# Performance work log

Hardware: AMD Instinct MI355X
Metric: run time of the kernel (lower is better)

## Reference

```python
import jax, jax.numpy as jnp
import numpy as np

B, L, D_MODEL = 8, 2048, 256
D_STATE, D_CONV, EXPAND, DT_RANK = 8, 4, 2, 2
D_INNER = EXPAND * D_MODEL
CHUNK = 32  # chunkSize in _parallelScan


def setup_inputs() -> dict:
    key = jax.random.key(0)
    ks = jax.random.split(key, 8)
    def nrm(k, shape, fan_in):
        return jax.random.normal(k, shape, jnp.float32) / np.float32(np.sqrt(fan_in))
    x = jax.random.normal(ks[0], (B, L, D_MODEL), jnp.float32)
    W_in = nrm(ks[1], (D_MODEL, 2 * D_INNER), D_MODEL)            # inProj (no bias)
    conv_w = nrm(ks[2], (D_INNER, 1, D_CONV), D_CONV)             # depthwise conv [O,I/g,K]
    conv_b = jnp.zeros((D_INNER,), jnp.float32)
    W_x = nrm(ks[3], (D_INNER, DT_RANK + 2 * D_STATE), D_INNER)   # xProj (no bias)
    dt_std = DT_RANK ** -0.5
    W_dt = jax.random.uniform(ks[4], (DT_RANK, D_INNER), jnp.float32, -dt_std, dt_std)
    u = jax.random.uniform(ks[5], (D_INNER,), jnp.float32)
    b_dt = u * np.float32(np.log(0.1) - np.log(0.001)) + np.float32(np.log(0.001))  # log(invDt)
    A_log = jnp.log(jnp.tile(jnp.arange(1, D_STATE + 1, dtype=jnp.float32), (D_INNER, 1)))
    Dp = jnp.ones((D_INNER,), jnp.float32)
    W_out = nrm(ks[6], (D_INNER, D_MODEL), D_INNER)
    pre_g = jnp.ones((D_MODEL,), jnp.float32)
    pre_b = jnp.zeros((D_MODEL,), jnp.float32)
    post_g = jnp.ones((D_MODEL,), jnp.float32)
    post_b = jnp.zeros((D_MODEL,), jnp.float32)
    return dict(x=x, pre_g=pre_g, pre_b=pre_b, post_g=post_g, post_b=post_b,
                W_in=W_in, conv_w=conv_w, conv_b=conv_b, W_x=W_x, W_dt=W_dt,
                b_dt=b_dt, A_log=A_log, Dp=Dp, W_out=W_out)


def layernorm(x, g, b, eps=1e-5):
    mu = jnp.mean(x, axis=-1, keepdims=True)
    var = jnp.var(x, axis=-1, keepdims=True)
    return (x - mu) * jax.lax.rsqrt(var + eps) * g + b


def _parallel_scan(deltaA, deltaBX, C, Dp, xc):
    # deltaA, deltaBX: [B, L, I, N]; C: [B, L, N]; xc: [B, L, I]
    Bb, Lb, I, N = deltaA.shape
    nC = Lb // CHUNK
    def chunked(t):
        return jnp.moveaxis(t.reshape((Bb, nC, CHUNK) + t.shape[2:]), 1, 0)
    cA, cBX, cC, cX = chunked(deltaA), chunked(deltaBX), chunked(C), chunked(xc)

    def body(h, inp):
        a, bx, c, xck = inp  # a,bx: [B,CHUNK,I,N]; c: [B,CHUNK,N]; xck: [B,CHUNK,I]
        logA = jnp.log(jnp.maximum(a, 1e-6))
        cum = jnp.cumsum(logA, axis=1)
        cumA = jnp.exp(jnp.minimum(cum, 20.0))
        hInit = h[:, None] * cumA
        inv = jnp.exp(-jnp.clip(cum, -20.0, 20.0))
        cumBX = jnp.cumsum(bx * inv, axis=1)
        hChunk = hInit + cumA * cumBX                      # [B,CHUNK,I,N]
        y = jnp.einsum('blin,bln->bli', hChunk, c) + xck * Dp
        return hChunk[:, -1], y

    h0 = jnp.zeros((Bb, I, N), deltaA.dtype)
    _, ys = jax.lax.scan(body, h0, (cA, cBX, cC, cX))      # ys: [nC,B,CHUNK,I]
    return jnp.moveaxis(ys, 0, 1).reshape(Bb, Lb, I)


def _ssm(x, W_in, conv_w, conv_b, W_x, W_dt, b_dt, A_log, Dp, W_out):
    Bb, Lb, _ = x.shape
    xr = x @ W_in                                          # [B,L,2I]
    xc, res = xr[..., :D_INNER], xr[..., D_INNER:]
    # depthwise causal conv (pad dConv-1 left == torch pad-both then slice [:L])
    xt = jnp.swapaxes(xc, 1, 2)                            # [B,I,L]
    xt = jax.lax.conv_general_dilated(
        xt, conv_w, window_strides=(1,), padding=[(D_CONV - 1, 0)],
        dimension_numbers=('NCH', 'OIH', 'NCH'), feature_group_count=D_INNER)
    xt = xt + conv_b[None, :, None]
    xc = jax.nn.silu(jnp.swapaxes(xt, 1, 2))               # [B,L,I]
    A = -jnp.exp(A_log.astype(jnp.float32))                # [I,N]
    xdbl = xc @ W_x
    delta = xdbl[..., :DT_RANK]
    Bm = xdbl[..., DT_RANK:DT_RANK + D_STATE]
    Cm = xdbl[..., DT_RANK + D_STATE:]
    delta = jax.nn.softplus(delta @ W_dt + b_dt)           # [B,L,I]
    deltaA = jnp.exp(delta[..., None] * A)                 # [B,L,I,N]
    deltaBX = delta[..., None] * Bm[:, :, None, :] * xc[..., None]
    y = _parallel_scan(deltaA, deltaBX, Cm, Dp.astype(jnp.float32), xc)
    y = y * jax.nn.silu(res)
    return y @ W_out


def reference(x, pre_g, pre_b, post_g, post_b, W_in, conv_w, conv_b, W_x, W_dt,
              b_dt, A_log, Dp, W_out):
    residual = x
    xn = layernorm(x, pre_g, pre_b)
    args = (W_in, conv_w, conv_b, W_x, W_dt, b_dt, A_log, Dp, W_out)
    h_fwd = _ssm(xn, *args)
    h_bwd = jnp.flip(_ssm(jnp.flip(xn, axis=1), *args), axis=1)
    out = residual + h_fwd + h_bwd                         # DropPath is identity (eval / p=0)
    return layernorm(out, post_g, post_b)
```

## Files before the change

### kernel.cpp

```cpp
#include <hip/hip_runtime.h>
#include <hip/hip_bf16.h>
#include <math.h>

#define BQ 8
#define LQ 2048
#define DM 256
#define DI 512
#define NS 8
#define NT (BQ*LQ)
#define NCH 64
#define CHK 32

typedef __attribute__((ext_vector_type(8))) __bf16 bf16x8;
typedef __attribute__((ext_vector_type(4))) float f32x4;

#define GPTR(p) ((const __attribute__((address_space(1))) void*)(p))
#define SPTR(p) ((__attribute__((address_space(3))) void*)(p))

__device__ __forceinline__ float fast_silu(float v){
  return v * __builtin_amdgcn_rcpf(1.0f + __expf(-v));
}
__device__ __forceinline__ unsigned short f2bf(float f){
  unsigned int u = __float_as_uint(f);
  unsigned int r = (u + 0x7FFFu + ((u >> 16) & 1u)) >> 16;
  return (unsigned short)r;
}
__device__ __forceinline__ float b2f(unsigned short u){
  return __uint_as_float(((unsigned int)u) << 16);
}
__device__ __forceinline__ f32x4 sp4(float x){ return (f32x4){x,x,x,x}; }

__global__ __launch_bounds__(256) void prep_kernel(const float* __restrict__ W_in,
                                                   const float* __restrict__ W_out,
                                                   const float* __restrict__ W_x,
                                                   unsigned short* __restrict__ WinT,
                                                   unsigned short* __restrict__ WoutT,
                                                   unsigned short* __restrict__ WxBC,
                                                   float* __restrict__ Wdt01){
  int id = blockIdx.x*256 + threadIdx.x;
  if(id < 1024*256){ int n = id >> 8, k = id & 255; WinT[id]  = f2bf(W_in[k*1024+n]); }
  if(id < 256*512){  int n = id >> 9, k = id & 511; WoutT[id] = f2bf(W_out[k*256+n]); }
  if(id < 16*512){   int j = id >> 9, k = id & 511; WxBC[id]  = f2bf(W_x[k*18+2+j]); }
  if(id < 2*512){    int j = id >> 9, k = id & 511; Wdt01[id] = W_x[k*18+j]; }
}

template<bool OB>
__global__ __launch_bounds__(256) void ln_kernel(const float* __restrict__ in,
                                                 const float* __restrict__ g,
                                                 const float* __restrict__ bv,
                                                 void* __restrict__ outp){
  int w = threadIdx.x >> 6, lane = threadIdx.x & 63;
  size_t row = (size_t)blockIdx.x*4 + w;
  const float4* rp = (const float4*)(in + row*DM);
  float4 v = rp[lane];
  float s  = v.x+v.y+v.z+v.w;
  float sq = v.x*v.x+v.y*v.y+v.z*v.z+v.w*v.w;
  #pragma unroll
  for(int m=32;m>=1;m>>=1){ s += __shfl_xor(s,m); sq += __shfl_xor(sq,m); }
  float mean = s*(1.0f/DM);
  float var  = sq*(1.0f/DM) - mean*mean;
  float rstd = rsqrtf(var + 1e-5f);
  float4 gv = ((const float4*)g)[lane];
  float4 bb = ((const float4*)bv)[lane];
  float4 o;
  o.x = (v.x-mean)*rstd*gv.x + bb.x;
  o.y = (v.y-mean)*rstd*gv.y + bb.y;
  o.z = (v.z-mean)*rstd*gv.z + bb.z;
  o.w = (v.w-mean)*rstd*gv.w + bb.w;
  if(OB){
    ushort4 q; q.x=f2bf(o.x); q.y=f2bf(o.y); q.z=f2bf(o.z); q.w=f2bf(o.w);
    *(ushort4*)((unsigned short*)outp + row*DM + lane*4) = q;
  } else {
    ((float4*)((float*)outp + row*DM))[lane] = o;
  }
}

template<int K, bool RESID, bool OUTBF>
__global__ __launch_bounds__(256) void gemm_bf16(const unsigned short* __restrict__ A,
                                                 const unsigned short* __restrict__ Bt,
                                                 const float* __restrict__ xres,
                                                 void* __restrict__ Cv, int N){
  __shared__ unsigned short As[128*32];
  __shared__ unsigned short Bs[128*32];
  const int tid = threadIdx.x;
  const int wid = tid >> 6, lane = tid & 63;
  const int wm = wid >> 1, wn = wid & 1;
  const int row0 = blockIdx.y*128, col0 = blockIdx.x*128;
  f32x4 acc[4][4] = {};

  for(int kt = 0; kt < K; kt += 32){
    {
      int ch = tid;
      const unsigned short* ga = A + (size_t)(row0 + (ch>>2))*K + kt + (ch&3)*8;
      __builtin_amdgcn_global_load_lds(GPTR(ga), SPTR(As + wid*512), 16, 0, 0);
      const unsigned short* gb = Bt + (size_t)(col0 + (ch>>2))*K + kt + (ch&3)*8;
      __builtin_amdgcn_global_load_lds(GPTR(gb), SPTR(Bs + wid*512), 16, 0, 0);
    }
    {
      int ch = tid + 256;
      const unsigned short* ga = A + (size_t)(row0 + (ch>>2))*K + kt + (ch&3)*8;
      __builtin_amdgcn_global_load_lds(GPTR(ga), SPTR(As + 2048 + wid*512), 16, 0, 0);
      const unsigned short* gb = Bt + (size_t)(col0 + (ch>>2))*K + kt + (ch&3)*8;
      __builtin_amdgcn_global_load_lds(GPTR(gb), SPTR(Bs + 2048 + wid*512), 16, 0, 0);
    }
    __syncthreads();

    bf16x8 af[4], bfv[4];
    #pragma unroll
    for(int m=0;m<4;m++)
      af[m] = *(const bf16x8*)(const void*)&As[(wm*64 + m*16 + (lane&15))*32 + (lane>>4)*8];
    #pragma unroll
    for(int n=0;n<4;n++)
      bfv[n] = *(const bf16x8*)(const void*)&Bs[(wn*64 + n*16 + (lane&15))*32 + (lane>>4)*8];
    #pragma unroll
    for(int m=0;m<4;m++)
      #pragma unroll
      for(int n=0;n<4;n++)
        acc[m][n] = __builtin_amdgcn_mfma_f32_16x16x32_bf16(af[m], bfv[n], acc[m][n], 0, 0, 0);
    __syncthreads();
  }

  const int cr = (lane>>4)*4, cc = lane&15;
  #pragma unroll
  for(int m=0;m<4;m++){
    #pragma unroll
    for(int n=0;n<4;n++){
      int col = col0 + wn*64 + n*16 + cc;
      size_t base = (size_t)(row0 + wm*64 + m*16 + cr)*N + col;
      #pragma unroll
      for(int r=0;r<4;r++){
        float v = acc[m][n][r];
        if constexpr (OUTBF){
          ((unsigned short*)Cv)[base + (size_t)r*N] = f2bf(v);
        } else {
          if constexpr (RESID) v += xres[base + (size_t)r*N];
          ((float*)Cv)[base + (size_t)r*N] = v;
        }
      }
    }
  }
}

__global__ __launch_bounds__(256) void conv_dt_kernel(const unsigned short* __restrict__ xrb,
                                                      const float* __restrict__ cw,
                                                      const float* __restrict__ cb,
                                                      const float* __restrict__ Wdt01,
                                                      float* __restrict__ xcf,
                                                      float* __restrict__ xcb,
                                                      unsigned short* __restrict__ xbf_f,
                                                      unsigned short* __restrict__ xbf_b,
                                                      float* __restrict__ dt2f,
                                                      float* __restrict__ dt2b){
  const int tid = threadIdx.x;
  const int tok = tid >> 7, q = tid & 127;
  const int i = q*4;
  const size_t row = (size_t)blockIdx.x*2 + tok;
  const int l = (int)(row & (LQ-1));

  float4 wc0 = *(const float4*)&cw[(i+0)*4];
  float4 wc1 = *(const float4*)&cw[(i+1)*4];
  float4 wc2 = *(const float4*)&cw[(i+2)*4];
  float4 wc3 = *(const float4*)&cw[(i+3)*4];
  float4 bias = *(const float4*)&cb[i];

  float4 r[7];
  #pragma unroll
  for(int d=0; d<7; d++){
    int off = d-3;
    bool ok = (l+off >= 0) && (l+off < LQ);
    if(ok){
      ushort4 t4 = *(const ushort4*)&xrb[(row+off)*1024 + i];
      r[d] = make_float4(b2f(t4.x), b2f(t4.y), b2f(t4.z), b2f(t4.w));
    } else r[d] = make_float4(0.f,0.f,0.f,0.f);
  }
  float4 sf = bias;
  sf.x += r[0].x*wc0.x + r[1].x*wc0.y + r[2].x*wc0.z + r[3].x*wc0.w;
  sf.y += r[0].y*wc1.x + r[1].y*wc1.y + r[2].y*wc1.z + r[3].y*wc1.w;
  sf.z += r[0].z*wc2.x + r[1].z*wc2.y + r[2].z*wc2.z + r[3].z*wc2.w;
  sf.w += r[0].w*wc3.x + r[1].w*wc3.y + r[2].w*wc3.z + r[3].w*wc3.w;
  float4 sb = bias;
  sb.x += r[6].x*wc0.x + r[5].x*wc0.y + r[4].x*wc0.z + r[3].x*wc0.w;
  sb.y += r[6].y*wc1.x + r[5].y*wc1.y + r[4].y*wc1.z + r[3].y*wc1.w;
  sb.z += r[6].z*wc2.x + r[5].z*wc2.y + r[4].z*wc2.z + r[3].z*wc2.w;
  sb.w += r[6].w*wc3.x + r[5].w*wc3.y + r[4].w*wc3.z + r[3].w*wc3.w;

  float4 of, ob;
  of.x = fast_silu(sf.x); of.y = fast_silu(sf.y); of.z = fast_silu(sf.z); of.w = fast_silu(sf.w);
  ob.x = fast_silu(sb.x); ob.y = fast_silu(sb.y); ob.z = fast_silu(sb.z); ob.w = fast_silu(sb.w);

  size_t e = row*512 + i;
  *(float4*)&xcf[e] = of;
  *(float4*)&xcb[e] = ob;
  ushort4 obf; obf.x=f2bf(of.x); obf.y=f2bf(of.y); obf.z=f2bf(of.z); obf.w=f2bf(of.w);
  *(ushort4*)&xbf_f[e] = obf;
  ushort4 obb; obb.x=f2bf(ob.x); obb.y=f2bf(ob.y); obb.z=f2bf(ob.z); obb.w=f2bf(ob.w);
  *(ushort4*)&xbf_b[e] = obb;

  float4 w0q = *(const float4*)&Wdt01[i];
  float4 w1q = *(const float4*)&Wdt01[512+i];
  float s0f = of.x*w0q.x + of.y*w0q.y + of.z*w0q.z + of.w*w0q.w;
  float s1f = of.x*w1q.x + of.y*w1q.y + of.z*w1q.z + of.w*w1q.w;
  float s0b = ob.x*w0q.x + ob.y*w0q.y + ob.z*w0q.z + ob.w*w0q.w;
  float s1b = ob.x*w1q.x + ob.y*w1q.y + ob.z*w1q.z + ob.w*w1q.w;
  #pragma unroll
  for(int m=32;m>=1;m>>=1){
    s0f += __shfl_xor(s0f,m); s1f += __shfl_xor(s1f,m);
    s0b += __shfl_xor(s0b,m); s1b += __shfl_xor(s1b,m);
  }
  __shared__ float red[4][4];
  int wid = tid >> 6;
  if((tid & 63) == 0){ red[wid][0]=s0f; red[wid][1]=s1f; red[wid][2]=s0b; red[wid][3]=s1b; }
  __syncthreads();
  if(tid == 0){
    size_t r0 = (size_t)blockIdx.x*2;
    dt2f[r0*2+0] = red[0][0]+red[1][0];  dt2f[r0*2+1] = red[0][1]+red[1][1];
    dt2b[r0*2+0] = red[0][2]+red[1][2];  dt2b[r0*2+1] = red[0][3]+red[1][3];
  }
  if(tid == 128){
    size_t r1 = (size_t)blockIdx.x*2 + 1;
    dt2f[r1*2+0] = red[2][0]+red[3][0];  dt2f[r1*2+1] = red[2][1]+red[3][1];
    dt2b[r1*2+0] = red[2][2]+red[3][2];  dt2b[r1*2+1] = red[2][3]+red[3][3];
  }
}

__global__ __launch_bounds__(256) void bc_gemm(const unsigned short* __restrict__ xbf_f,
                                               const unsigned short* __restrict__ xbf_b,
                                               const unsigned short* __restrict__ WxBC,
                                               float* __restrict__ BCf,
                                               float* __restrict__ BCb){
  int dir = blockIdx.y;
  const unsigned short* A = dir ? xbf_b : xbf_f;
  float* BC = dir ? BCb : BCf;
  const int row0 = blockIdx.x*256;
  __shared__ unsigned short As[256*32];
  __shared__ unsigned short Bs[16*32];
  const int tid = threadIdx.x, wid = tid>>6, lane = tid&63;
  f32x4 acc[4] = {};
  for(int kt=0; kt<512; kt+=32){
    #pragma unroll
    for(int r=0;r<4;r++){
      int ch = r*256 + tid;
      const unsigned short* ga = A + (size_t)(row0 + (ch>>2))*512 + kt + (ch&3)*8;
      __builtin_amdgcn_global_load_lds(GPTR(ga), SPTR(As + r*2048 + wid*512), 16, 0, 0);
    }
    if(wid==0){
      int ch = lane;
      const unsigned short* gb = WxBC + (size_t)(ch>>2)*512 + kt + (ch&3)*8;
      __builtin_amdgcn_global_load_lds(GPTR(gb), SPTR(Bs), 16, 0, 0);
    }
    __syncthreads();
    bf16x8 bfv = *(const bf16x8*)(const void*)&Bs[(lane&15)*32 + (lane>>4)*8];
    #pragma unroll
    for(int m=0;m<4;m++){
      bf16x8 af = *(const bf16x8*)(const void*)&As[(wid*64 + m*16 + (lane&15))*32 + (lane>>4)*8];
      acc[m] = __builtin_amdgcn_mfma_f32_16x16x32_bf16(af, bfv, acc[m], 0, 0, 0);
    }
    __syncthreads();
  }
  const int cr = (lane>>4)*4, cc = lane&15;
  #pragma unroll
  for(int m=0;m<4;m++)
    #pragma unroll
    for(int r=0;r<4;r++)
      BC[(size_t)(row0 + wid*64 + m*16 + cr + r)*16 + cc] = acc[m][r];
}

#define INV_CAP  4.85165195e8f

__global__ __launch_bounds__(256) void scan_pass1(
    const float* __restrict__ dt2f, const float* __restrict__ dt2b,
    const float* __restrict__ BCf,  const float* __restrict__ BCb,
    const float* __restrict__ xcf,  const float* __restrict__ xcb,
    const float* __restrict__ Wdt,  const float* __restrict__ bdt,
    float* __restrict__ a_arr, float* __restrict__ b_arr){
  int dir = blockIdx.z, b = blockIdx.y;
  int chunk = blockIdx.x >> 1, ib = blockIdx.x & 1;
  int i = ib*256 + threadIdx.x;
  const float* dt2 = dir ? dt2b : dt2f;
  const float* BC  = dir ? BCb  : BCf;
  const float* xc  = dir ? xcb  : xcf;
  float w0 = Wdt[i], w1 = Wdt[512+i], bd = bdt[i];
  f32x4 cAA = sp4(1.f), cAB = sp4(1.f), ivA = sp4(1.f), ivB = sp4(1.f);
  f32x4 cxA = sp4(0.f), cxB = sp4(0.f);
  for(int t=0;t<CHK;t++){
    int p = chunk*CHK + t;
    int l = dir ? (LQ-1-p) : p;
    size_t row = (size_t)b*LQ + l;
    float d0 = dt2[row*2+0], d1 = dt2[row*2+1];
    float dpre = d0*w0 + d1*w1 + bd;
    float t0 = __expf(fminf(dpre, 80.f));
    float ep = 1.f + t0;
    float e1 = __builtin_amdgcn_rcpf(ep);
    float delta = __logf(ep);
    float dxv = delta * xc[row*512+i];
    const f32x4* bc4 = (const f32x4*)&BC[row*16];
    f32x4 bmA = bc4[0], bmB = bc4[1];
    float e2=e1*e1, e4=e2*e2;
    f32x4 pdA = {e1, e2, e2*e1, e4};
    f32x4 pdB = pdA * e4;
    float g2=ep*ep, g4=g2*g2;
    f32x4 puA = {ep, g2, g2*ep, g4};
    f32x4 puB = puA * g4;
    cAA *= __builtin_elementwise_max(pdA, sp4(1e-6f));
    cAB *= __builtin_elementwise_max(pdB, sp4(1e-6f));
    ivA *= __builtin_elementwise_min(puA, sp4(1e6f));
    ivB *= __builtin_elementwise_min(puB, sp4(1e6f));
    f32x4 iuA = __builtin_elementwise_min(ivA, sp4(INV_CAP));
    f32x4 iuB = __builtin_elementwise_min(ivB, sp4(INV_CAP));
    cxA += (bmA * iuA) * dxv;
    cxB += (bmB * iuB) * dxv;
  }
  size_t base = (size_t)((dir*BQ + b)*NCH + chunk)*4096 + i;
  f32x4 bA = cAA*cxA, bB = cAB*cxB;
  #pragma unroll
  for(int n=0;n<4;n++){
    a_arr[base + n*512]       = cAA[n];
    a_arr[base + (n+4)*512]   = cAB[n];
    b_arr[base + n*512]       = bA[n];
    b_arr[base + (n+4)*512]   = bB[n];
  }
}

__global__ __launch_bounds__(256) void scan_pass2(float* __restrict__ a_arr,
                                                  const float* __restrict__ b_arr){
  int dir = blockIdx.z, b = blockIdx.y;
  int j = blockIdx.x*256 + threadIdx.x;
  size_t base = (size_t)(dir*BQ + b)*NCH*4096 + j;
  float h = 0.f;
  for(int c=0;c<NCH;c++){
    size_t idx = base + (size_t)c*4096;
    float a = a_arr[idx], bb = b_arr[idx];
    a_arr[idx] = h;
    h = a*h + bb;
  }
}

__global__ __launch_bounds__(128) void scan_pass3z(
    const float* __restrict__ dt2f, const float* __restrict__ dt2b,
    const float* __restrict__ BCf,  const float* __restrict__ BCb,
    const float* __restrict__ xcf,  const float* __restrict__ xcb,
    const unsigned short* __restrict__ xrb,
    const float* __restrict__ Wdt,  const float* __restrict__ bdt,
    const float* __restrict__ Dpv,  const float* __restrict__ hin,
    unsigned short* __restrict__ z){
  __shared__ float yfs[CHK][128];
  int b = blockIdx.y;
  int c = blockIdx.x >> 2, ic = blockIdx.x & 3;
  int tid = threadIdx.x;
  int i = ic*128 + tid;
  float w0 = Wdt[i], w1 = Wdt[512+i], bd = bdt[i], dp = Dpv[i];

  {
    size_t base = (size_t)(((size_t)b)*NCH + c)*4096 + i;
    f32x4 hqA = {hin[base+0*512], hin[base+1*512], hin[base+2*512], hin[base+3*512]};
    f32x4 hqB = {hin[base+4*512], hin[base+5*512], hin[base+6*512], hin[base+7*512]};
    f32x4 cAA = sp4(1.f), cAB = sp4(1.f), ivA = sp4(1.f), ivB = sp4(1.f);
    for(int t=0;t<CHK;t++){
      size_t row = (size_t)b*LQ + c*CHK + t;
      float d0 = dt2f[row*2+0], d1 = dt2f[row*2+1];
      float dpre = d0*w0 + d1*w1 + bd;
      float t0 = __expf(fminf(dpre, 80.f));
      float ep = 1.f + t0;
      float e1 = __builtin_amdgcn_rcpf(ep);
      float delta = __logf(ep);
      float xv = xcf[row*512+i];
      float dxv = delta*xv;
      const f32x4* bc4 = (const f32x4*)&BCf[row*16];
      f32x4 bmA = bc4[0], bmB = bc4[1], cmA = bc4[2], cmB = bc4[3];
      float e2=e1*e1, e4=e2*e2;
      f32x4 pdA = {e1, e2, e2*e1, e4};
      f32x4 pdB = pdA * e4;
      float g2=ep*ep, g4=g2*g2;
      f32x4 puA = {ep, g2, g2*ep, g4};
      f32x4 puB = puA * g4;
      cAA *= __builtin_elementwise_max(pdA, sp4(1e-6f));
      cAB *= __builtin_elementwise_max(pdB, sp4(1e-6f));
      ivA *= __builtin_elementwise_min(puA, sp4(1e6f));
      ivB *= __builtin_elementwise_min(puB, sp4(1e6f));
      f32x4 iuA = __builtin_elementwise_min(ivA, sp4(INV_CAP));
      f32x4 iuB = __builtin_elementwise_min(ivB, sp4(INV_CAP));
      hqA += (bmA * iuA) * dxv;
      hqB += (bmB * iuB) * dxv;
      f32x4 yv = (cAA*hqA)*cmA + (cAB*hqB)*cmB;
      yfs[t][tid] = xv*dp + yv[0] + yv[1] + yv[2] + yv[3];
    }
  }
  {
    int cb_ = NCH-1-c;
    size_t base = (size_t)(((size_t)BQ + b)*NCH + cb_)*4096 + i;
    f32x4 hqA = {hin[base+0*512], hin[base+1*512], hin[base+2*512], hin[base+3*512]};
    f32x4 hqB = {hin[base+4*512], hin[base+5*512], hin[base+6*512], hin[base+7*512]};
    f32x4 cAA = sp4(1.f), cAB = sp4(1.f), ivA = sp4(1.f), ivB = sp4(1.f);
    for(int t=0;t<CHK;t++){
      int l = c*CHK + (CHK-1-t);
      size_t row = (size_t)b*LQ + l;
      float d0 = dt2b[row*2+0], d1 = dt2b[row*2+1];
      float dpre = d0*w0 + d1*w1 + bd;
      float t0 = __expf(fminf(dpre, 80.f));
      float ep = 1.f + t0;
      float e1 = __builtin_amdgcn_rcpf(ep);
      float delta = __logf(ep);
      float xv = xcb[row*512+i];
      float dxv = delta*xv;
      const f32x4* bc4 = (const f32x4*)&BCb[row*16];
      f32x4 bmA = bc4[0], bmB = bc4[1], cmA = bc4[2], cmB = bc4[3];
      float e2=e1*e1, e4=e2*e2;
      f32x4 pdA = {e1, e2, e2*e1, e4};
      f32x4 pdB = pdA * e4;
      float g2=ep*ep, g4=g2*g2;
      f32x4 puA = {ep, g2, g2*ep, g4};
      f32x4 puB = puA * g4;
      cAA *= __builtin_elementwise_max(pdA, sp4(1e-6f));
      cAB *= __builtin_elementwise_max(pdB, sp4(1e-6f));
      ivA *= __builtin_elementwise_min(puA, sp4(1e6f));
      ivB *= __builtin_elementwise_min(puB, sp4(1e6f));
      f32x4 iuA = __builtin_elementwise_min(ivA, sp4(INV_CAP));
      f32x4 iuB = __builtin_elementwise_min(ivB, sp4(INV_CAP));
      hqA += (bmA * iuA) * dxv;
      hqB += (bmB * iuB) * dxv;
      f32x4 yv = (cAA*hqA)*cmA + (cAB*hqB)*cmB;
      float yb = xv*dp + yv[0] + yv[1] + yv[2] + yv[3];
      float yf = yfs[CHK-1-t][tid];
      float res = b2f(xrb[row*1024 + 512 + i]);
      z[row*512 + i] = f2bf((yf + yb) * fast_silu(res));
    }
  }
}

extern "C" void kernel_launch(void* const* d_in, const int* in_sizes, int n_in,
                              void* d_out, int out_size, void* d_ws, size_t ws_size,
                              hipStream_t stream) {
  const float* x      = (const float*)d_in[0];
  const float* pre_g  = (const float*)d_in[1];
  const float* pre_b  = (const float*)d_in[2];
  const float* post_g = (const float*)d_in[3];
  const float* post_b = (const float*)d_in[4];
  const float* W_in   = (const float*)d_in[5];
  const float* conv_w = (const float*)d_in[6];
  const float* conv_b = (const float*)d_in[7];
  const float* W_x    = (const float*)d_in[8];
  const float* W_dt   = (const float*)d_in[9];
  const float* b_dt   = (const float*)d_in[10];
  const float* Dp     = (const float*)d_in[12];
  const float* W_out  = (const float*)d_in[13];
  float* out = (float*)d_out;

  float* ws    = (float*)d_ws;
  float* xr32  = ws;
  unsigned short* xr_bf = (unsigned short*)xr32;
  float* xn32  = xr32  + (size_t)NT*1024;
  float* xcf   = xn32  + (size_t)NT*256;
  float* xcb   = xcf   + (size_t)NT*512;
  float* dt2f  = xcb   + (size_t)NT*512;
  float* dt2b  = dt2f  + (size_t)NT*2;
  float* BCf   = dt2b  + (size_t)NT*2;
  float* BCb   = BCf   + (size_t)NT*16;
  float* a_arr = BCb   + (size_t)NT*16;
  float* b_arr = a_arr + (size_t)2*BQ*NCH*NS*DI;
  unsigned short* WinT  = (unsigned short*)(b_arr + (size_t)2*BQ*NCH*NS*DI);
  unsigned short* WoutT = WinT + 1024*256;
  unsigned short* WxBC  = WoutT + 256*512;
  float* Wdt01          = (float*)(WxBC + 16*512);
  unsigned short* xn_bf  = (unsigned short*)a_arr;
  unsigned short* xbf_f  = (unsigned short*)a_arr;
  unsigned short* xbf_b  = (unsigned short*)b_arr;
  unsigned short* z_bf   = (unsigned short*)b_arr;

  prep_kernel<<<1024, 256, 0, stream>>>(W_in, W_out, W_x, WinT, WoutT, WxBC, Wdt01);
  ln_kernel<true><<<NT/4, 256, 0, stream>>>(x, pre_g, pre_b, xn_bf);
  gemm_bf16<256,false,true><<<dim3(1024/128, NT/128), 256, 0, stream>>>(xn_bf, WinT, nullptr, xr_bf, 1024);
  conv_dt_kernel<<<NT/2, 256, 0, stream>>>(xr_bf, conv_w, conv_b, Wdt01,
                                           xcf, xcb, xbf_f, xbf_b, dt2f, dt2b);
  bc_gemm<<<dim3(NT/256, 2), 256, 0, stream>>>(xbf_f, xbf_b, WxBC, BCf, BCb);
  scan_pass1<<<dim3(NCH*2, BQ, 2), 256, 0, stream>>>(dt2f, dt2b, BCf, BCb, xcf, xcb,
                                                     W_dt, b_dt, a_arr, b_arr);
  scan_pass2<<<dim3(16, BQ, 2), 256, 0, stream>>>(a_arr, b_arr);
  scan_pass3z<<<dim3(NCH*4, BQ), 128, 0, stream>>>(dt2f, dt2b, BCf, BCb, xcf, xcb, xr_bf,
                                                   W_dt, b_dt, Dp, a_arr, z_bf);
  gemm_bf16<512,true,false><<<dim3(256/128, NT/128), 256, 0, stream>>>(z_bf, WoutT, x, xn32, 256);
  ln_kernel<false><<<NT/4, 256, 0, stream>>>(xn32, post_g, post_b, out);
}
```

Before: 208.0 us.

## Drop fp32 conv outputs, read bf16 in scans, and reformulate chunk scan recurrence

The conv kernel no longer writes fp32 copies of the conv/SiLU output, and both scan passes read the existing bf16 copies instead, which cuts global memory traffic. Inside the chunk scans, the inverse-cumprod accumulation (tracking both the cumulative product and its capped inverse) is replaced by a direct recurrence S = a*S + w*B*dx with a clamp weight, so the per-step upward products are no longer computed. The scan loops are also unrolled by two. Reading x in bf16 lowers the precision of the scan inputs, and the clamp-weight formulation only approximately reproduces the reference's capped log-space behaviour.

```diff
diff --git a/kernel.cpp b/kernel.cpp
--- a/kernel.cpp
+++ b/kernel.cpp
@@ -29,6 +29,8 @@
   return __uint_as_float(((unsigned int)u) << 16);
 }
 __device__ __forceinline__ f32x4 sp4(float x){ return (f32x4){x,x,x,x}; }
+
+#define E20F  4.85165195e8f
 
 __global__ __launch_bounds__(256) void prep_kernel(const float* __restrict__ W_in,
                                                    const float* __restrict__ W_out,
@@ -145,8 +147,6 @@
                                                       const float* __restrict__ cw,
                                                       const float* __restrict__ cb,
                                                       const float* __restrict__ Wdt01,
-                                                      float* __restrict__ xcf,
-                                                      float* __restrict__ xcb,
                                                       unsigned short* __restrict__ xbf_f,
                                                       unsigned short* __restrict__ xbf_b,
                                                       float* __restrict__ dt2f,
@@ -189,8 +189,6 @@
   ob.x = fast_silu(sb.x); ob.y = fast_silu(sb.y); ob.z = fast_silu(sb.z); ob.w = fast_silu(sb.w);
 
   size_t e = row*512 + i;
-  *(float4*)&xcf[e] = of;
-  *(float4*)&xcb[e] = ob;
   ushort4 obf; obf.x=f2bf(of.x); obf.y=f2bf(of.y); obf.z=f2bf(of.z); obf.w=f2bf(of.w);
   *(ushort4*)&xbf_f[e] = obf;
   ushort4 obb; obb.x=f2bf(ob.x); obb.y=f2bf(ob.y); obb.z=f2bf(ob.z); obb.w=f2bf(ob.w);
@@ -265,12 +263,11 @@
       BC[(size_t)(row0 + wid*64 + m*16 + cr + r)*16 + cc] = acc[m][r];
 }
 
-#define INV_CAP  4.85165195e8f
 
 __global__ __launch_bounds__(256) void scan_pass1(
     const float* __restrict__ dt2f, const float* __restrict__ dt2b,
     const float* __restrict__ BCf,  const float* __restrict__ BCb,
-    const float* __restrict__ xcf,  const float* __restrict__ xcb,
+    const unsigned short* __restrict__ xbf_f, const unsigned short* __restrict__ xbf_b,
     const float* __restrict__ Wdt,  const float* __restrict__ bdt,
     float* __restrict__ a_arr, float* __restrict__ b_arr){
   int dir = blockIdx.z, b = blockIdx.y;
@@ -278,10 +275,10 @@
   int i = ib*256 + threadIdx.x;
   const float* dt2 = dir ? dt2b : dt2f;
   const float* BC  = dir ? BCb  : BCf;
-  const float* xc  = dir ? xcb  : xcf;
+  const unsigned short* xc = dir ? xbf_b : xbf_f;
   float w0 = Wdt[i], w1 = Wdt[512+i], bd = bdt[i];
-  f32x4 cAA = sp4(1.f), cAB = sp4(1.f), ivA = sp4(1.f), ivB = sp4(1.f);
-  f32x4 cxA = sp4(0.f), cxB = sp4(0.f);
+  f32x4 cAA = sp4(1.f), cAB = sp4(1.f), SA = sp4(0.f), SB = sp4(0.f);
+  #pragma unroll 2
   for(int t=0;t<CHK;t++){
     int p = chunk*CHK + t;
     int l = dir ? (LQ-1-p) : p;
@@ -292,32 +289,27 @@
     float ep = 1.f + t0;
     float e1 = __builtin_amdgcn_rcpf(ep);
     float delta = __logf(ep);
-    float dxv = delta * xc[row*512+i];
+    float dxv = delta * b2f(xc[row*512+i]);
     const f32x4* bc4 = (const f32x4*)&BC[row*16];
     f32x4 bmA = bc4[0], bmB = bc4[1];
     float e2=e1*e1, e4=e2*e2;
     f32x4 pdA = {e1, e2, e2*e1, e4};
     f32x4 pdB = pdA * e4;
-    float g2=ep*ep, g4=g2*g2;
-    f32x4 puA = {ep, g2, g2*ep, g4};
-    f32x4 puB = puA * g4;
-    cAA *= __builtin_elementwise_max(pdA, sp4(1e-6f));
-    cAB *= __builtin_elementwise_max(pdB, sp4(1e-6f));
-    ivA *= __builtin_elementwise_min(puA, sp4(1e6f));
-    ivB *= __builtin_elementwise_min(puB, sp4(1e6f));
-    f32x4 iuA = __builtin_elementwise_min(ivA, sp4(INV_CAP));
-    f32x4 iuB = __builtin_elementwise_min(ivB, sp4(INV_CAP));
-    cxA += (bmA * iuA) * dxv;
-    cxB += (bmB * iuB) * dxv;
+    f32x4 emA = __builtin_elementwise_max(pdA, sp4(1e-6f));
+    f32x4 emB = __builtin_elementwise_max(pdB, sp4(1e-6f));
+    cAA *= emA;  cAB *= emB;
+    f32x4 wA = __builtin_elementwise_min(cAA*E20F, sp4(1.f));
+    f32x4 wB = __builtin_elementwise_min(cAB*E20F, sp4(1.f));
+    SA = emA*SA + (bmA*wA)*dxv;
+    SB = emB*SB + (bmB*wB)*dxv;
   }
   size_t base = (size_t)((dir*BQ + b)*NCH + chunk)*4096 + i;
-  f32x4 bA = cAA*cxA, bB = cAB*cxB;
   #pragma unroll
   for(int n=0;n<4;n++){
-    a_arr[base + n*512]       = cAA[n];
-    a_arr[base + (n+4)*512]   = cAB[n];
-    b_arr[base + n*512]       = bA[n];
-    b_arr[base + (n+4)*512]   = bB[n];
+    a_arr[base + n*512]     = cAA[n];
+    a_arr[base + (n+4)*512] = cAB[n];
+    b_arr[base + n*512]     = SA[n];
+    b_arr[base + (n+4)*512] = SB[n];
   }
 }
 
@@ -338,7 +330,7 @@
 __global__ __launch_bounds__(128) void scan_pass3z(
     const float* __restrict__ dt2f, const float* __restrict__ dt2b,
     const float* __restrict__ BCf,  const float* __restrict__ BCb,
-    const float* __restrict__ xcf,  const float* __restrict__ xcb,
+    const unsigned short* __restrict__ xbf_f, const unsigned short* __restrict__ xbf_b,
     const unsigned short* __restrict__ xrb,
     const float* __restrict__ Wdt,  const float* __restrict__ bdt,
     const float* __restrict__ Dpv,  const float* __restrict__ hin,
@@ -352,9 +344,10 @@
 
   {
     size_t base = (size_t)(((size_t)b)*NCH + c)*4096 + i;
-    f32x4 hqA = {hin[base+0*512], hin[base+1*512], hin[base+2*512], hin[base+3*512]};
-    f32x4 hqB = {hin[base+4*512], hin[base+5*512], hin[base+6*512], hin[base+7*512]};
-    f32x4 cAA = sp4(1.f), cAB = sp4(1.f), ivA = sp4(1.f), ivB = sp4(1.f);
+    f32x4 h0A = {hin[base+0*512], hin[base+1*512], hin[base+2*512], hin[base+3*512]};
+    f32x4 h0B = {hin[base+4*512], hin[base+5*512], hin[base+6*512], hin[base+7*512]};
+    f32x4 cAA = sp4(1.f), cAB = sp4(1.f), SA = sp4(0.f), SB = sp4(0.f);
+    #pragma unroll 2
     for(int t=0;t<CHK;t++){
       size_t row = (size_t)b*LQ + c*CHK + t;
       float d0 = dt2f[row*2+0], d1 = dt2f[row*2+1];
@@ -363,34 +356,31 @@
       float ep = 1.f + t0;
       float e1 = __builtin_amdgcn_rcpf(ep);
       float delta = __logf(ep);
-      float xv = xcf[row*512+i];
+      float xv = b2f(xbf_f[row*512+i]);
       float dxv = delta*xv;
       const f32x4* bc4 = (const f32x4*)&BCf[row*16];
       f32x4 bmA = bc4[0], bmB = bc4[1], cmA = bc4[2], cmB = bc4[3];
       float e2=e1*e1, e4=e2*e2;
       f32x4 pdA = {e1, e2, e2*e1, e4};
       f32x4 pdB = pdA * e4;
-      float g2=ep*ep, g4=g2*g2;
-      f32x4 puA = {ep, g2, g2*ep, g4};
-      f32x4 puB = puA * g4;
-      cAA *= __builtin_elementwise_max(pdA, sp4(1e-6f));
-      cAB *= __builtin_elementwise_max(pdB, sp4(1e-6f));
-      ivA *= __builtin_elementwise_min(puA, sp4(1e6f));
-      ivB *= __builtin_elementwise_min(puB, sp4(1e6f));
-      f32x4 iuA = __builtin_elementwise_min(ivA, sp4(INV_CAP));
-      f32x4 iuB = __builtin_elementwise_min(ivB, sp4(INV_CAP));
-      hqA += (bmA * iuA) * dxv;
-      hqB += (bmB * iuB) * dxv;
-      f32x4 yv = (cAA*hqA)*cmA + (cAB*hqB)*cmB;
+      f32x4 emA = __builtin_elementwise_max(pdA, sp4(1e-6f));
+      f32x4 emB = __builtin_elementwise_max(pdB, sp4(1e-6f));
+      cAA *= emA;  cAB *= emB;
+      f32x4 wA = __builtin_elementwise_min(cAA*E20F, sp4(1.f));
+      f32x4 wB = __builtin_elementwise_min(cAB*E20F, sp4(1.f));
+      SA = emA*SA + (bmA*wA)*dxv;
+      SB = emB*SB + (bmB*wB)*dxv;
+      f32x4 yv = (cAA*h0A + SA)*cmA + (cAB*h0B + SB)*cmB;
       yfs[t][tid] = xv*dp + yv[0] + yv[1] + yv[2] + yv[3];
     }
   }
   {
     int cb_ = NCH-1-c;
     size_t base = (size_t)(((size_t)BQ + b)*NCH + cb_)*4096 + i;
-    f32x4 hqA = {hin[base+0*512], hin[base+1*512], hin[base+2*512], hin[base+3*512]};
-    f32x4 hqB = {hin[base+4*512], hin[base+5*512], hin[base+6*512], hin[base+7*512]};
-    f32x4 cAA = sp4(1.f), cAB = sp4(1.f), ivA = sp4(1.f), ivB = sp4(1.f);
+    f32x4 h0A = {hin[base+0*512], hin[base+1*512], hin[base+2*512], hin[base+3*512]};
+    f32x4 h0B = {hin[base+4*512], hin[base+5*512], hin[base+6*512], hin[base+7*512]};
+    f32x4 cAA = sp4(1.f), cAB = sp4(1.f), SA = sp4(0.f), SB = sp4(0.f);
+    #pragma unroll 2
     for(int t=0;t<CHK;t++){
       int l = c*CHK + (CHK-1-t);
       size_t row = (size_t)b*LQ + l;
@@ -400,25 +390,21 @@
       float ep = 1.f + t0;
       float e1 = __builtin_amdgcn_rcpf(ep);
       float delta = __logf(ep);
-      float xv = xcb[row*512+i];
+      float xv = b2f(xbf_b[row*512+i]);
       float dxv = delta*xv;
       const f32x4* bc4 = (const f32x4*)&BCb[row*16];
       f32x4 bmA = bc4[0], bmB = bc4[1], cmA = bc4[2], cmB = bc4[3];
       float e2=e1*e1, e4=e2*e2;
       f32x4 pdA = {e1, e2, e2*e1, e4};
       f32x4 pdB = pdA * e4;
-      float g2=ep*ep, g4=g2*g2;
-      f32x4 puA = {ep, g2, g2*ep, g4};
-      f32x4 puB = puA * g4;
-      cAA *= __builtin_elementwise_max(pdA, sp4(1e-6f));
-      cAB *= __builtin_elementwise_max(pdB, sp4(1e-6f));
-      ivA *= __builtin_elementwise_min(puA, sp4(1e6f));
-      ivB *= __builtin_elementwise_min(puB, sp4(1e6f));
-      f32x4 iuA = __builtin_elementwise_min(ivA, sp4(INV_CAP));
-      f32x4 iuB = __builtin_elementwise_min(ivB, sp4(INV_CAP));
-      hqA += (bmA * iuA) * dxv;
-      hqB += (bmB * iuB) * dxv;
-      f32x4 yv = (cAA*hqA)*cmA + (cAB*hqB)*cmB;
+      f32x4 emA = __builtin_elementwise_max(pdA, sp4(1e-6f));
+      f32x4 emB = __builtin_elementwise_max(pdB, sp4(1e-6f));
+      cAA *= emA;  cAB *= emB;
+      f32x4 wA = __builtin_elementwise_min(cAA*E20F, sp4(1.f));
+      f32x4 wB = __builtin_elementwise_min(cAB*E20F, sp4(1.f));
+      SA = emA*SA + (bmA*wA)*dxv;
+      SB = emB*SB + (bmB*wB)*dxv;
+      f32x4 yv = (cAA*h0A + SA)*cmA + (cAB*h0B + SB)*cmB;
       float yb = xv*dp + yv[0] + yv[1] + yv[2] + yv[3];
       float yf = yfs[CHK-1-t][tid];
       float res = b2f(xrb[row*1024 + 512 + i]);
@@ -449,9 +435,11 @@
   float* xr32  = ws;
   unsigned short* xr_bf = (unsigned short*)xr32;
   float* xn32  = xr32  + (size_t)NT*1024;
-  float* xcf   = xn32  + (size_t)NT*256;
-  float* xcb   = xcf   + (size_t)NT*512;
-  float* dt2f  = xcb   + (size_t)NT*512;
+  float* xcfr  = xn32  + (size_t)NT*256;
+  unsigned short* xbf_f = (unsigned short*)xcfr;
+  float* xcbr  = xcfr  + (size_t)NT*512;
+  unsigned short* xbf_b = (unsigned short*)xcbr;
+  float* dt2f  = xcbr  + (size_t)NT*512;
   float* dt2b  = dt2f  + (size_t)NT*2;
   float* BCf   = dt2b  + (size_t)NT*2;
   float* BCb   = BCf   + (size_t)NT*16;
@@ -461,21 +449,19 @@
   unsigned short* WoutT = WinT + 1024*256;
   unsigned short* WxBC  = WoutT + 256*512;
   float* Wdt01          = (float*)(WxBC + 16*512);
-  unsigned short* xn_bf  = (unsigned short*)a_arr;
-  unsigned short* xbf_f  = (unsigned short*)a_arr;
-  unsigned short* xbf_b  = (unsigned short*)b_arr;
-  unsigned short* z_bf   = (unsigned short*)b_arr;
+  unsigned short* xn_bf = (unsigned short*)a_arr;
+  unsigned short* z_bf  = (unsigned short*)b_arr;
 
   prep_kernel<<<1024, 256, 0, stream>>>(W_in, W_out, W_x, WinT, WoutT, WxBC, Wdt01);
   ln_kernel<true><<<NT/4, 256, 0, stream>>>(x, pre_g, pre_b, xn_bf);
   gemm_bf16<256,false,true><<<dim3(1024/128, NT/128), 256, 0, stream>>>(xn_bf, WinT, nullptr, xr_bf, 1024);
   conv_dt_kernel<<<NT/2, 256, 0, stream>>>(xr_bf, conv_w, conv_b, Wdt01,
-                                           xcf, xcb, xbf_f, xbf_b, dt2f, dt2b);
+                                           xbf_f, xbf_b, dt2f, dt2b);
   bc_gemm<<<dim3(NT/256, 2), 256, 0, stream>>>(xbf_f, xbf_b, WxBC, BCf, BCb);
-  scan_pass1<<<dim3(NCH*2, BQ, 2), 256, 0, stream>>>(dt2f, dt2b, BCf, BCb, xcf, xcb,
+  scan_pass1<<<dim3(NCH*2, BQ, 2), 256, 0, stream>>>(dt2f, dt2b, BCf, BCb, xbf_f, xbf_b,
                                                      W_dt, b_dt, a_arr, b_arr);
   scan_pass2<<<dim3(16, BQ, 2), 256, 0, stream>>>(a_arr, b_arr);
-  scan_pass3z<<<dim3(NCH*4, BQ), 128, 0, stream>>>(dt2f, dt2b, BCf, BCb, xcf, xcb, xr_bf,
+  scan_pass3z<<<dim3(NCH*4, BQ), 128, 0, stream>>>(dt2f, dt2b, BCf, BCb, xbf_f, xbf_b, xr_bf,
                                                    W_dt, b_dt, Dp, a_arr, z_bf);
   gemm_bf16<512,true,false><<<dim3(256/128, NT/128), 256, 0, stream>>>(z_bf, WoutT, x, xn32, 256);
   ln_kernel<false><<<NT/4, 256, 0, stream>>>(xn32, post_g, post_b, out);
```

Result: faster. 187.4 us (-9.9%).
